# Kernel tuning notes

Hardware: AMD Instinct MI355X
Metric: run time of the kernel (lower is better)

## Reference

```python
import jax, jax.numpy as jnp
import numpy as np
from jax import lax

C = 256
POOL = 7
NUM_CLASSES = 81
D = NUM_CLASSES - 1
STRIDES = (4, 8, 16, 32)
DEC_MULT = (0.1, 0.1, 0.2, 0.2)  # decode_settings: multipliers on raw deltas
LOG_MAX = float(np.log(1000.0 / 16.0))


def setup_inputs() -> dict:
    key = jax.random.key(0)
    ks = jax.random.split(key, 16)
    n, Rp = 2, 512
    R = n * Rp
    img = 800.0
    cx = jax.random.uniform(ks[0], (R,), minval=0.0, maxval=img)
    cy = jax.random.uniform(ks[1], (R,), minval=0.0, maxval=img)
    w = jax.random.uniform(ks[2], (R,), minval=16.0, maxval=300.0)
    h = jax.random.uniform(ks[3], (R,), minval=16.0, maxval=300.0)
    x1 = jnp.clip(cx - w / 2, 0.0, img - 1.0)
    y1 = jnp.clip(cy - h / 2, 0.0, img - 1.0)
    x2 = jnp.minimum(jnp.maximum(cx + w / 2, x1 + 1.0), img)
    y2 = jnp.minimum(jnp.maximum(cy + h / 2, y1 + 1.0), img)
    proposals = jnp.stack([x1, y1, x2, y2], -1)
    imidx = jnp.repeat(jnp.arange(n, dtype=jnp.int32), Rp)
    fmaps = {}
    for li, s in enumerate(STRIDES):
        hw = int(800 // s)
        fmaps[f"fmap{li}"] = jax.random.normal(ks[4 + li], (n, hw, hw, C), jnp.float32)
    c1, clin = C * POOL * POOL, 1024
    def lin(k, fi, fo):
        return (jax.random.normal(k, (fi, fo), jnp.float32) / np.sqrt(fi).astype(np.float32),
                jnp.zeros((fo,), jnp.float32))
    W0, b0 = lin(ks[8], c1, clin)
    W1, b1 = lin(ks[9], clin, clin)
    Wc, bc = lin(ks[10], clin, NUM_CLASSES)
    Wr, br = lin(ks[11], clin, NUM_CLASSES * 4)
    imsizes = jnp.full((n, 2), img, jnp.float32)  # (h, w) per image
    return dict(proposals=proposals, imidx=imidx, **fmaps,
                W0=W0, b0=b0, W1=W1, b1=b1, Wc=Wc, bc=bc, Wr=Wr, br=br,
                imsizes=imsizes, score_thr=0.05, iou_thr=0.5, imtop=100, min_size=1.0)


def _roi_align_level(fmap, boxes, imidx, stride):
    # fmap [n,H,W,C], boxes [R,4] xyxy in image coords; 1 sample per bin, bilinear.
    n, H, W, c = fmap.shape
    s = 1.0 / stride
    x1, y1, x2, y2 = boxes[:, 0] * s, boxes[:, 1] * s, boxes[:, 2] * s, boxes[:, 3] * s
    g = (jnp.arange(POOL, dtype=jnp.float32) + 0.5) / POOL  # bin centers in [0,1]
    xs = x1[:, None] + g[None, :] * (x2 - x1)[:, None] - 0.5  # [R,POOL]
    ys = y1[:, None] + g[None, :] * (y2 - y1)[:, None] - 0.5
    R = boxes.shape[0]
    xx = jnp.broadcast_to(xs[:, None, :], (R, POOL, POOL))
    yy = jnp.broadcast_to(ys[:, :, None], (R, POOL, POOL))
    x0f, y0f = jnp.floor(xx), jnp.floor(yy)
    wx, wy = xx - x0f, yy - y0f
    x0 = jnp.clip(x0f.astype(jnp.int32), 0, W - 1)
    x1i = jnp.clip(x0f.astype(jnp.int32) + 1, 0, W - 1)
    y0 = jnp.clip(y0f.astype(jnp.int32), 0, H - 1)
    y1i = jnp.clip(y0f.astype(jnp.int32) + 1, 0, H - 1)
    ii = imidx[:, None, None]
    v00 = fmap[ii, y0, x0]; v01 = fmap[ii, y0, x1i]
    v10 = fmap[ii, y1i, x0]; v11 = fmap[ii, y1i, x1i]  # each [R,POOL,POOL,C]
    wx, wy = wx[..., None], wy[..., None]
    return (v00 * (1 - wx) * (1 - wy) + v01 * wx * (1 - wy)
            + v10 * (1 - wx) * wy + v11 * wx * wy)


def _forward(proposals, imidx, fmaps, W0, b0, W1, b1, Wc, bc, Wr, br,
             imsizes, score_thr, iou_thr, imtop, min_size):
    R = proposals.shape[0]
    pw = proposals[:, 2] - proposals[:, 0]
    ph = proposals[:, 3] - proposals[:, 1]
    # FPN level assignment (torchvision canonical formula)
    lvl = jnp.floor(4.0 + jnp.log2(jnp.sqrt(pw * ph) / 224.0 + 1e-6))
    lvl = jnp.clip(lvl, 2, 5).astype(jnp.int32) - 2
    pooled = jnp.zeros((R, POOL, POOL, C), fmaps[0].dtype)
    for k, (fm, st) in enumerate(zip(fmaps, STRIDES)):
        pk = _roi_align_level(fm, proposals, imidx, st)
        pooled = jnp.where((lvl == k)[:, None, None, None], pk, pooled)
    # two-FC head + cls/reg
    x = pooled.reshape(R, -1)
    x = jax.nn.relu(x @ W0 + b0)
    x = jax.nn.relu(x @ W1 + b1)
    reg = (x @ Wr + br).reshape(R, NUM_CLASSES, 4)[:, 1:]      # [R,D,4]
    scr = jax.nn.softmax(x @ Wc + bc, axis=-1)[:, 1:]          # [R,D]
    cls = jnp.broadcast_to(jnp.arange(1, NUM_CLASSES, dtype=jnp.int32), (R, D))
    # decode boxes (proposal cwh + weighted deltas, log-space clamp)
    cx = (proposals[:, 0] + proposals[:, 2]) * 0.5
    cy = (proposals[:, 1] + proposals[:, 3]) * 0.5
    dx = reg[..., 0] * DEC_MULT[0]
    dy = reg[..., 1] * DEC_MULT[1]
    dw = jnp.minimum(reg[..., 2] * DEC_MULT[2], LOG_MAX)
    dh = jnp.minimum(reg[..., 3] * DEC_MULT[3], LOG_MAX)
    ncx = dx * pw[:, None] + cx[:, None]
    ncy = dy * ph[:, None] + cy[:, None]
    nw = jnp.exp(dw) * pw[:, None]
    nh = jnp.exp(dh) * ph[:, None]
    hb = imsizes[imidx, 0][:, None]
    wb = imsizes[imidx, 1][:, None]
    bx1 = jnp.clip(ncx - nw / 2, 0.0, wb); bx2 = jnp.clip(ncx + nw / 2, 0.0, wb)
    by1 = jnp.clip(ncy - nh / 2, 0.0, hb); by2 = jnp.clip(ncy + nh / 2, 0.0, hb)
    boxes = jnp.stack([bx1, by1, bx2, by2], -1)                # [R,D,4]
    valid = (scr > score_thr) & (bx2 - bx1 >= min_size) & (by2 - by1 >= min_size)
    # flatten roi-class pairs; class-offset boxes = torchvision batched_nms trick
    M = R * D
    boxes_f = boxes.reshape(M, 4)
    scr_f = scr.reshape(M)
    cls_f = cls.reshape(M)
    valid_f = valid.reshape(M)
    imidx_f = jnp.repeat(imidx, D)
    off = cls_f.astype(boxes_f.dtype)[:, None] * (jnp.max(imsizes) + 2.0)
    bo = boxes_f + off
    areas = (bo[:, 2] - bo[:, 0]) * (bo[:, 3] - bo[:, 1])
    def nms(scores0):
        def step(scores, _):
            i = jnp.argmax(scores)
            s = scores[i]
            b = bo[i]
            iw = jnp.clip(jnp.minimum(b[2], bo[:, 2]) - jnp.maximum(b[0], bo[:, 0]), 0.0)
            ih = jnp.clip(jnp.minimum(b[3], bo[:, 3]) - jnp.maximum(b[1], bo[:, 1]), 0.0)
            inter = iw * ih
            iou = inter / (areas[i] + areas - inter + 1e-6)
            scores = jnp.where(iou > iou_thr, -1.0, scores)
            scores = scores.at[i].set(-1.0)
            return scores, (i, s)
        _, (idx, s) = lax.scan(step, scores0, None, length=imtop)
        return idx, s
    n = imsizes.shape[0]
    ob, osc, ocl = [], [], []
    for i in range(n):
        s0 = jnp.where(valid_f & (imidx_f == i), scr_f, -1.0)
        idx, s = nms(s0)
        keep = s > 0.0  # padded slots have score <= 0
        ob.append(jnp.where(keep[:, None], boxes_f[idx], 0.0))
        osc.append(jnp.where(keep, s, 0.0))
        ocl.append(jnp.where(keep, cls_f[idx], -1))
    return jnp.stack(ob), jnp.stack(osc), jnp.stack(ocl)


def reference(proposals, imidx, fmap0, fmap1, fmap2, fmap3, W0, b0, W1, b1,
              Wc, bc, Wr, br, imsizes, score_thr, iou_thr, imtop, min_size):
    return _forward(proposals, imidx, (fmap0, fmap1, fmap2, fmap3), W0, b0, W1,
                    b1, Wc, bc, Wr, br, imsizes, score_thr, iou_thr, int(imtop),
                    min_size)
```

## Files before the change

kernel.cpp:

```cpp
#include <hip/hip_runtime.h>
#include <math.h>

#define CCH 256
#define NPOOL 7
#define NCLS 81
#define DCLS 80
#define NHEAD 512
#define FLOG_MAX 4.1351666f

typedef _Float16 half8 __attribute__((ext_vector_type(8)));
typedef _Float16 half4 __attribute__((ext_vector_type(4)));
typedef float floatx4 __attribute__((ext_vector_type(4)));

__global__ void zero_k(float4* __restrict__ p, int count4)
{
    int i = blockIdx.x * blockDim.x + threadIdx.x;
    if (i < count4) p[i] = make_float4(0.f, 0.f, 0.f, 0.f);
}

__device__ __forceinline__ void roi_setup(
    const float* __restrict__ prop, const int* __restrict__ imidx,
    const float* __restrict__ f0, const float* __restrict__ f1,
    const float* __restrict__ f2, const float* __restrict__ f3,
    int h0, int h1, int h2, int h3, int b,
    const float*& base, int& W, size_t& o00, size_t& o01, size_t& o10, size_t& o11,
    float& w00, float& w01, float& w10, float& w11)
{
    int roi = b / 49, p = b % 49;
    int py = p / 7, px = p % 7;

    const float* pr = prop + (size_t)roi * 4;
    float x1 = pr[0], y1 = pr[1], x2 = pr[2], y2 = pr[3];
    float pw = x2 - x1, ph = y2 - y1;

    float lv = floorf(4.0f + log2f(sqrtf(pw * ph) / 224.0f + 1e-6f));
    lv = fminf(fmaxf(lv, 2.0f), 5.0f);
    int lvl = (int)lv - 2;

    const float* fm; int H; float s;
    if (lvl == 0)      { fm = f0; H = h0; s = 0.25f;    }
    else if (lvl == 1) { fm = f1; H = h1; s = 0.125f;   }
    else if (lvl == 2) { fm = f2; H = h2; s = 0.0625f;  }
    else               { fm = f3; H = h3; s = 0.03125f; }
    W = H;

    float xs1 = x1 * s, ys1 = y1 * s, xs2 = x2 * s, ys2 = y2 * s;
    float gx = (px + 0.5f) / 7.0f, gy = (py + 0.5f) / 7.0f;
    float xx = xs1 + gx * (xs2 - xs1) - 0.5f;
    float yy = ys1 + gy * (ys2 - ys1) - 0.5f;
    float x0f = floorf(xx), y0f = floorf(yy);
    float wx = xx - x0f, wy = yy - y0f;
    int x0i = min(max((int)x0f, 0), W - 1);
    int x1i = min(max((int)x0f + 1, 0), W - 1);
    int y0i = min(max((int)y0f, 0), H - 1);
    int y1i = min(max((int)y0f + 1, 0), H - 1);

    int ii = imidx[roi];
    base = fm + (size_t)ii * H * W * CCH;
    o00 = ((size_t)y0i * W + x0i) * CCH;
    o01 = ((size_t)y0i * W + x1i) * CCH;
    o10 = ((size_t)y1i * W + x0i) * CCH;
    o11 = ((size_t)y1i * W + x1i) * CCH;
    w00 = (1.0f - wx) * (1.0f - wy);
    w01 = wx * (1.0f - wy);
    w10 = (1.0f - wx) * wy;
    w11 = wx * wy;
}

__global__ void roi_align_k(const float* __restrict__ prop,
                            const int* __restrict__ imidx,
                            const float* __restrict__ f0,
                            const float* __restrict__ f1,
                            const float* __restrict__ f2,
                            const float* __restrict__ f3,
                            int h0, int h1, int h2, int h3,
                            float* __restrict__ pooled)
{
    int b = blockIdx.x, c = threadIdx.x;
    const float* base; int W; size_t o00, o01, o10, o11;
    float w00, w01, w10, w11;
    roi_setup(prop, imidx, f0, f1, f2, f3, h0, h1, h2, h3, b,
              base, W, o00, o01, o10, o11, w00, w01, w10, w11);
    float v = base[o00 + c] * w00 + base[o01 + c] * w01
            + base[o10 + c] * w10 + base[o11 + c] * w11;
    pooled[(size_t)b * CCH + c] = v;
}

__global__ __launch_bounds__(256) void roi_align_f16v4_k(
    const float* __restrict__ prop, const int* __restrict__ imidx,
    const float* __restrict__ f0, const float* __restrict__ f1,
    const float* __restrict__ f2, const float* __restrict__ f3,
    int h0, int h1, int h2, int h3,
    _Float16* __restrict__ poolH, _Float16* __restrict__ poolL)
{
    int b = blockIdx.x * 4 + (threadIdx.x >> 6);
    int lane = threadIdx.x & 63;
    const float* base; int W; size_t o00, o01, o10, o11;
    float w00, w01, w10, w11;
    roi_setup(prop, imidx, f0, f1, f2, f3, h0, h1, h2, h3, b,
              base, W, o00, o01, o10, o11, w00, w01, w10, w11);

    int c4 = lane * 4;
    float4 v00 = *(const float4*)(base + o00 + c4);
    float4 v01 = *(const float4*)(base + o01 + c4);
    float4 v10 = *(const float4*)(base + o10 + c4);
    float4 v11 = *(const float4*)(base + o11 + c4);
    const float* p00 = (const float*)&v00;
    const float* p01 = (const float*)&v01;
    const float* p10 = (const float*)&v10;
    const float* p11 = (const float*)&v11;

    half4 h, l;
#pragma unroll
    for (int e = 0; e < 4; ++e) {
        float v = p00[e] * w00 + p01[e] * w01 + p10[e] * w10 + p11[e] * w11;
        _Float16 hh = (_Float16)v;
        h[e] = hh;
        l[e] = (_Float16)(v - (float)hh);
    }
    size_t idx = (size_t)b * CCH + c4;
    *(half4*)(poolH + idx) = h;
    *(half4*)(poolL + idx) = l;
}

__global__ __launch_bounds__(256) void convert_w_t_k(const float* __restrict__ W,
                                                     _Float16* __restrict__ WtH,
                                                     _Float16* __restrict__ WtL,
                                                     int K, int N)
{
    __shared__ float sh[64][65];
    int k0 = blockIdx.x * 64, n0 = blockIdx.y * 64;
    int t = threadIdx.x;
#pragma unroll
    for (int p = 0; p < 4; ++p) {
        int idx = p * 256 + t;
        int kr = idx >> 4, nc = (idx & 15) * 4;
        float4 v = *(const float4*)(W + (size_t)(k0 + kr) * N + n0 + nc);
        sh[kr][nc + 0] = v.x; sh[kr][nc + 1] = v.y;
        sh[kr][nc + 2] = v.z; sh[kr][nc + 3] = v.w;
    }
    __syncthreads();
#pragma unroll
    for (int p = 0; p < 4; ++p) {
        int idx = p * 256 + t;
        int nr = idx >> 4, kc = (idx & 15) * 4;
        half4 h, l;
#pragma unroll
        for (int i = 0; i < 4; ++i) {
            float v = sh[kc + i][nr];
            _Float16 hh = (_Float16)v;
            h[i] = hh;
            l[i] = (_Float16)(v - (float)hh);
        }
        *(half4*)(WtH + (size_t)(n0 + nr) * K + k0 + kc) = h;
        *(half4*)(WtL + (size_t)(n0 + nr) * K + k0 + kc) = l;
    }
}

__global__ __launch_bounds__(256) void convert_w_t_guard_k(const float* __restrict__ W,
                                                           _Float16* __restrict__ WtH,
                                                           _Float16* __restrict__ WtL,
                                                           int K, int N, int Kt, int rowofs)
{
    __shared__ float sh[64][65];
    int k0 = blockIdx.x * 64, n0 = blockIdx.y * 64;
    int t = threadIdx.x;
#pragma unroll
    for (int p = 0; p < 4; ++p) {
        int idx = p * 256 + t;
        int kr = idx >> 4, nc = (idx & 15) * 4;
#pragma unroll
        for (int e = 0; e < 4; ++e) {
            int nn = n0 + nc + e;
            sh[kr][nc + e] = (nn < N) ? W[(size_t)(k0 + kr) * N + nn] : 0.0f;
        }
    }
    __syncthreads();
#pragma unroll
    for (int p = 0; p < 4; ++p) {
        int idx = p * 256 + t;
        int nr = idx >> 4, kc = (idx & 15) * 4;
        if (n0 + nr < N) {
            half4 h, l;
#pragma unroll
            for (int i = 0; i < 4; ++i) {
                float v = sh[kc + i][nr];
                _Float16 hh = (_Float16)v;
                h[i] = hh;
                l[i] = (_Float16)(v - (float)hh);
            }
            *(half4*)(WtH + (size_t)(rowofs + n0 + nr) * Kt + k0 + kc) = h;
            *(half4*)(WtL + (size_t)(rowofs + n0 + nr) * Kt + k0 + kc) = l;
        }
    }
}

__global__ void act_split_k(const float* __restrict__ acc,
                            const float* __restrict__ bias,
                            _Float16* __restrict__ outH,
                            _Float16* __restrict__ outL,
                            int total, int CL)
{
    int i = (blockIdx.x * blockDim.x + threadIdx.x) * 4;
    if (i >= total) return;
    int b = i % CL;
    float4 v = *(const float4*)(acc + i);
    float4 bb = *(const float4*)(bias + b);
    const float* pv = (const float*)&v;
    const float* pb = (const float*)&bb;
    half4 h, l;
#pragma unroll
    for (int e = 0; e < 4; ++e) {
        float f = fmaxf(pv[e] + pb[e], 0.0f);
        _Float16 hh = (_Float16)f;
        h[e] = hh;
        l[e] = (_Float16)(f - (float)hh);
    }
    *(half4*)(outH + i) = h;
    *(half4*)(outL + i) = l;
}

__device__ __forceinline__ void dma16(const _Float16* g, _Float16* l)
{
    __builtin_amdgcn_global_load_lds(
        (const __attribute__((address_space(1))) unsigned int*)g,
        (__attribute__((address_space(3))) unsigned int*)l, 16, 0, 0);
}

#define LDKE 32

__global__ __launch_bounds__(256) void gemm_mfma_split_k(
    const _Float16* __restrict__ Ah, const _Float16* __restrict__ Al,
    const _Float16* __restrict__ Bh, const _Float16* __restrict__ Bl,
    float* __restrict__ Cacc, int M, int N, int K, int Kc, int SP)
{
    __shared__ _Float16 sAh[128 * LDKE], sAl[128 * LDKE];
    __shared__ _Float16 sBh[128 * LDKE], sBl[128 * LDKE];

    int bid = blockIdx.x;
    int z = bid % SP;
    int q = bid / SP;
    int NT = N >> 7;
    int nn = q % NT;
    int m = q / NT;
    int m0 = m * 128, n0 = nn * 128;
    int kb = z * Kc;
    int ke = min(K, kb + Kc);

    int t = threadIdx.x;
    int lane = t & 63, w = t >> 6;
    int wr = w >> 1, wc = w & 1;
    int fr = lane & 15;
    int fk = (lane >> 4) * 8;

    int drow = w * 32 + (lane >> 2);
    int dkq = (lane & 3) * 8;
    const _Float16* gAh = Ah + (size_t)(m0 + drow) * K + dkq;
    const _Float16* gAl = Al + (size_t)(m0 + drow) * K + dkq;
    const _Float16* gBh = Bh + (size_t)(n0 + drow) * K + dkq;
    const _Float16* gBl = Bl + (size_t)(n0 + drow) * K + dkq;
    size_t rowskip = (size_t)16 * K;

    _Float16* lAh0 = &sAh[(w * 2 + 0) * 512];
    _Float16* lAh1 = &sAh[(w * 2 + 1) * 512];
    _Float16* lAl0 = &sAl[(w * 2 + 0) * 512];
    _Float16* lAl1 = &sAl[(w * 2 + 1) * 512];
    _Float16* lBh0 = &sBh[(w * 2 + 0) * 512];
    _Float16* lBh1 = &sBh[(w * 2 + 1) * 512];
    _Float16* lBl0 = &sBl[(w * 2 + 0) * 512];
    _Float16* lBl1 = &sBl[(w * 2 + 1) * 512];

    floatx4 acc[4][4] = {};

    for (int k0 = kb; k0 < ke; k0 += 32) {
        dma16(gAh + k0, lAh0);
        dma16(gAh + rowskip + k0, lAh1);
        dma16(gAl + k0, lAl0);
        dma16(gAl + rowskip + k0, lAl1);
        dma16(gBh + k0, lBh0);
        dma16(gBh + rowskip + k0, lBh1);
        dma16(gBl + k0, lBl0);
        dma16(gBl + rowskip + k0, lBl1);
        __syncthreads();

        half8 ah[4], al[4], bh[4], bl[4];
#pragma unroll
        for (int i = 0; i < 4; ++i) {
            int ar = wr * 64 + i * 16 + fr;
            ah[i] = *(const half8*)&sAh[ar * LDKE + fk];
            al[i] = *(const half8*)&sAl[ar * LDKE + fk];
            int bc = wc * 64 + i * 16 + fr;
            bh[i] = *(const half8*)&sBh[bc * LDKE + fk];
            bl[i] = *(const half8*)&sBl[bc * LDKE + fk];
        }
#pragma unroll
        for (int i = 0; i < 4; ++i)
#pragma unroll
            for (int j = 0; j < 4; ++j) {
                acc[i][j] = __builtin_amdgcn_mfma_f32_16x16x32_f16(ah[i], bh[j], acc[i][j], 0, 0, 0);
                acc[i][j] = __builtin_amdgcn_mfma_f32_16x16x32_f16(ah[i], bl[j], acc[i][j], 0, 0, 0);
                acc[i][j] = __builtin_amdgcn_mfma_f32_16x16x32_f16(al[i], bh[j], acc[i][j], 0, 0, 0);
            }
        __syncthreads();
    }

    int rbase = (lane >> 4) * 4;
#pragma unroll
    for (int i = 0; i < 4; ++i)
#pragma unroll
        for (int j = 0; j < 4; ++j) {
            int col = n0 + wc * 64 + j * 16 + fr;
#pragma unroll
            for (int r = 0; r < 4; ++r) {
                int row = m0 + wr * 64 + i * 16 + rbase + r;
                atomicAdd(&Cacc[(size_t)row * N + col], acc[i][j][r]);
            }
        }
}

__global__ __launch_bounds__(256) void gemm_mfma_fused64_k(
    const _Float16* __restrict__ Ah, const _Float16* __restrict__ Al,
    const _Float16* __restrict__ Bh, const _Float16* __restrict__ Bl,
    const float* __restrict__ bias,
    float* __restrict__ Cout,
    _Float16* __restrict__ outH, _Float16* __restrict__ outL,
    int M, int N, int K, int mode)
{
    __shared__ _Float16 sAh[2][64 * LDKE], sAl[2][64 * LDKE];
    __shared__ _Float16 sBh[2][64 * LDKE], sBl[2][64 * LDKE];

    int m0 = blockIdx.y * 64, n0 = blockIdx.x * 64;
    int t = threadIdx.x;
    int lane = t & 63, w = t >> 6;
    int wr = w >> 1, wc = w & 1;
    int fr = lane & 15;
    int fk = (lane >> 4) * 8;

    int drow = w * 16 + (lane >> 2);
    int dkq = (lane & 3) * 8;
    const _Float16* gAh = Ah + (size_t)(m0 + drow) * K + dkq;
    const _Float16* gAl = Al + (size_t)(m0 + drow) * K + dkq;
    const _Float16* gBh = Bh + (size_t)(n0 + drow) * K + dkq;
    const _Float16* gBl = Bl + (size_t)(n0 + drow) * K + dkq;
    int lofs = w * 512;

    int nt = K >> 5;

    dma16(gAh + 0, &sAh[0][lofs]);
    dma16(gAl + 0, &sAl[0][lofs]);
    dma16(gBh + 0, &sBh[0][lofs]);
    dma16(gBl + 0, &sBl[0][lofs]);
    __syncthreads();

    floatx4 acc[2][2] = {};

    for (int tt = 0; tt < nt; ++tt) {
        int c = tt & 1, nb = c ^ 1;
        if (tt + 1 < nt) {
            int k1 = (tt + 1) << 5;
            dma16(gAh + k1, &sAh[nb][lofs]);
            dma16(gAl + k1, &sAl[nb][lofs]);
            dma16(gBh + k1, &sBh[nb][lofs]);
            dma16(gBl + k1, &sBl[nb][lofs]);
        }

        half8 ah[2], av[2], bh[2], bv[2];
#pragma unroll
        for (int i = 0; i < 2; ++i) {
            int ar = wr * 32 + i * 16 + fr;
            ah[i] = *(const half8*)&sAh[c][ar * LDKE + fk];
            av[i] = *(const half8*)&sAl[c][ar * LDKE + fk];
            int bc = wc * 32 + i * 16 + fr;
            bh[i] = *(const half8*)&sBh[c][bc * LDKE + fk];
            bv[i] = *(const half8*)&sBl[c][bc * LDKE + fk];
        }
#pragma unroll
        for (int i = 0; i < 2; ++i)
#pragma unroll
            for (int j = 0; j < 2; ++j) {
                acc[i][j] = __builtin_amdgcn_mfma_f32_16x16x32_f16(ah[i], bh[j], acc[i][j], 0, 0, 0);
                acc[i][j] = __builtin_amdgcn_mfma_f32_16x16x32_f16(ah[i], bv[j], acc[i][j], 0, 0, 0);
                acc[i][j] = __builtin_amdgcn_mfma_f32_16x16x32_f16(av[i], bh[j], acc[i][j], 0, 0, 0);
            }
        __syncthreads();
    }

    int rbase = (lane >> 4) * 4;
#pragma unroll
    for (int i = 0; i < 2; ++i)
#pragma unroll
        for (int j = 0; j < 2; ++j) {
            int col = n0 + wc * 32 + j * 16 + fr;
#pragma unroll
            for (int r = 0; r < 4; ++r) {
                int row = m0 + wr * 32 + i * 16 + rbase + r;
                float v = acc[i][j][r];
                if (mode == 0) {
                    Cout[(size_t)row * N + col] = v;
                } else {
                    float f = fmaxf(v + bias[col], 0.0f);
                    _Float16 hh = (_Float16)f;
                    outH[(size_t)row * N + col] = hh;
                    outL[(size_t)row * N + col] = (_Float16)(f - (float)hh);
                }
            }
        }
}

__global__ __launch_bounds__(256) void gemm_splitk_k(const float* __restrict__ A,
                                                     const float* __restrict__ B,
                                                     const float* __restrict__ abias,
                                                     float* __restrict__ Cacc,
                                                     int M, int N, int K, int Kc)
{
    __shared__ float Ast[16][68];
    __shared__ float Bs[16][68];

    int m0 = blockIdx.y * 64, n0 = blockIdx.x * 64;
    int kb = blockIdx.z * Kc;
    int ke = min(K, kb + Kc);
    int tid = threadIdx.x;
    int tx = tid & 15, ty = tid >> 4;
    int arow = tid >> 2, akq = (tid & 3) << 2;
    int bcol = tid & 63, bk = tid >> 6;

    const float* Arow = A + (size_t)(m0 + arow) * K;
    bool nfull = (n0 + 64 <= N);

    float acc[4][4] = {};

    for (int k0 = kb; k0 < ke; k0 += 16) {
        float4 av = *(const float4*)(Arow + k0 + akq);
        if (abias) {
            av.x = fmaxf(av.x + abias[k0 + akq + 0], 0.0f);
            av.y = fmaxf(av.y + abias[k0 + akq + 1], 0.0f);
            av.z = fmaxf(av.z + abias[k0 + akq + 2], 0.0f);
            av.w = fmaxf(av.w + abias[k0 + akq + 3], 0.0f);
        }
        float bv[4];
        if (nfull) {
#pragma unroll
            for (int e = 0; e < 4; ++e)
                bv[e] = B[(size_t)(k0 + bk * 4 + e) * N + n0 + bcol];
        } else {
            bool ok = (n0 + bcol) < N;
#pragma unroll
            for (int e = 0; e < 4; ++e)
                bv[e] = ok ? B[(size_t)(k0 + bk * 4 + e) * N + n0 + bcol] : 0.0f;
        }
        __syncthreads();
        Ast[akq + 0][arow] = av.x;
        Ast[akq + 1][arow] = av.y;
        Ast[akq + 2][arow] = av.z;
        Ast[akq + 3][arow] = av.w;
#pragma unroll
        for (int e = 0; e < 4; ++e) Bs[bk * 4 + e][bcol] = bv[e];
        __syncthreads();

#pragma unroll
        for (int kk = 0; kk < 16; ++kk) {
            float4 af = *(const float4*)&Ast[kk][ty * 4];
            float4 bf = *(const float4*)&Bs[kk][tx * 4];
            float a_[4] = {af.x, af.y, af.z, af.w};
            float b_[4] = {bf.x, bf.y, bf.z, bf.w};
#pragma unroll
            for (int i = 0; i < 4; ++i)
#pragma unroll
                for (int j = 0; j < 4; ++j)
                    acc[i][j] = fmaf(a_[i], b_[j], acc[i][j]);
        }
    }

#pragma unroll
    for (int i = 0; i < 4; ++i) {
        int row = m0 + ty * 4 + i;
#pragma unroll
        for (int j = 0; j < 4; ++j) {
            int col = n0 + tx * 4 + j;
            if (col < N) atomicAdd(&Cacc[(size_t)row * N + col], acc[i][j]);
        }
    }
}

__global__ void softmax_k(const float* __restrict__ logits, int ldl,
                          const float* __restrict__ bc,
                          float* __restrict__ scr)
{
    int r = blockIdx.x;
    int t = threadIdx.x;
    const float* row = logits + (size_t)r * ldl;

    float v0 = row[t] + bc[t];
    float v1 = (t + 64 < NCLS) ? (row[t + 64] + bc[t + 64]) : -INFINITY;
    float m = fmaxf(v0, v1);
#pragma unroll
    for (int o = 32; o > 0; o >>= 1) m = fmaxf(m, __shfl_down(m, o));
    m = __shfl(m, 0);

    float e0 = expf(v0 - m);
    float e1 = (t + 64 < NCLS) ? expf(v1 - m) : 0.0f;
    float sum = e0 + e1;
#pragma unroll
    for (int o = 32; o > 0; o >>= 1) sum += __shfl_down(sum, o);
    sum = __shfl(sum, 0);
    float inv = 1.0f / sum;

    if (t >= 1)        scr[(size_t)r * DCLS + (t - 1)]  = e0 * inv;
    if (t + 64 < NCLS) scr[(size_t)r * DCLS + (t + 63)] = e1 * inv;
}

#define NMS_T 1024
#define NMS_CPT 8
__global__ __launch_bounds__(NMS_T) void nms_k(
    const float* __restrict__ scr,
    const float* __restrict__ prop,
    const int* __restrict__ imidx,
    const float* __restrict__ head, int ldh, int regofs,
    const float* __restrict__ br,
    const float* __restrict__ imsz,
    const float* __restrict__ score_thr_p,
    const float* __restrict__ min_size_p,
    const float* __restrict__ iou_thr_p,
    int* __restrict__ cidx,
    float* __restrict__ cscore,
    float* __restrict__ cbo,
    float* __restrict__ cbox,
    float* __restrict__ carea,
    float* __restrict__ out,
    int M, int n, int imtop)
{
    int img = blockIdx.x;
    int t = threadIdx.x;
    const int T = NMS_T;
    const int NW = NMS_T / 64;
    int lane = t & 63, wid = t >> 6;

    __shared__ int cnt;
    __shared__ float ws_sc[NW], ws_o0[NW], ws_o1[NW], ws_o2[NW], ws_o3[NW], ws_ar[NW];
    __shared__ int ws_g[NW], ws_p[NW];
    __shared__ float f_sc, f_o0, f_o1, f_o2, f_o3, f_ar;
    __shared__ int f_g, f_p;

    if (t == 0) cnt = 0;
    __syncthreads();

    float score_thr = score_thr_p[0];
    float min_size  = min_size_p[0];
    float iou_thr   = iou_thr_p[0];
    float immax = imsz[0];
    for (int q = 1; q < 2 * n; ++q) immax = fmaxf(immax, imsz[q]);

    int base = img * M;
    for (int j = t; j < M; j += T) {
        int r = j / DCLS;
        if (imidx[r] != img) continue;
        float s = scr[j];
        if (s <= score_thr) continue;

        int cls = j - r * DCLS + 1;
        const float* pr = prop + (size_t)r * 4;
        float pw = pr[2] - pr[0], ph = pr[3] - pr[1];
        float cx = (pr[0] + pr[2]) * 0.5f, cy = (pr[1] + pr[3]) * 0.5f;
        const float* rg_ = head + (size_t)r * ldh + regofs + cls * 4;
        const float* bb = br + cls * 4;
        float dx = (rg_[0] + bb[0]) * 0.1f;
        float dy = (rg_[1] + bb[1]) * 0.1f;
        float dw = fminf((rg_[2] + bb[2]) * 0.2f, FLOG_MAX);
        float dh = fminf((rg_[3] + bb[3]) * 0.2f, FLOG_MAX);
        float ncx = dx * pw + cx;
        float ncy = dy * ph + cy;
        float nw = expf(dw) * pw;
        float nh = expf(dh) * ph;
        float hbound = imsz[img * 2 + 0];
        float wbound = imsz[img * 2 + 1];
        float bx1 = fminf(fmaxf(ncx - nw * 0.5f, 0.0f), wbound);
        float bx2 = fminf(fmaxf(ncx + nw * 0.5f, 0.0f), wbound);
        float by1 = fminf(fmaxf(ncy - nh * 0.5f, 0.0f), hbound);
        float by2 = fminf(fmaxf(ncy + nh * 0.5f, 0.0f), hbound);
        if (bx2 - bx1 < min_size || by2 - by1 < min_size) continue;

        float off = (float)cls * (immax + 2.0f);
        int p = atomicAdd(&cnt, 1);
        cidx[base + p] = j;
        cscore[base + p] = s;
        cbox[(size_t)(base + p) * 4 + 0] = bx1;
        cbox[(size_t)(base + p) * 4 + 1] = by1;
        cbox[(size_t)(base + p) * 4 + 2] = bx2;
        cbox[(size_t)(base + p) * 4 + 3] = by2;
        cbo[(size_t)(base + p) * 4 + 0] = bx1 + off;
        cbo[(size_t)(base + p) * 4 + 1] = by1 + off;
        cbo[(size_t)(base + p) * 4 + 2] = bx2 + off;
        cbo[(size_t)(base + p) * 4 + 3] = by2 + off;
        carea[base + p] = (bx2 - bx1) * (by2 - by1);
    }
    __syncthreads();
    int K = cnt;

    float* ob  = out;
    float* osc = out + (size_t)n * imtop * 4;
    float* ocl = out + (size_t)n * imtop * 5;

    int it = 0;
    if (K <= T * NMS_CPT) {
        float rsc[NMS_CPT], ro0[NMS_CPT], ro1[NMS_CPT], ro2[NMS_CPT], ro3[NMS_CPT], rar[NMS_CPT];
        int rgi[NMS_CPT];
#pragma unroll
        for (int s = 0; s < NMS_CPT; ++s) {
            int p = t + s * T;
            bool ok = p < K;
            rsc[s] = ok ? cscore[base + p] : -1e30f;
            rgi[s] = ok ? cidx[base + p] : 0x7fffffff;
            ro0[s] = ok ? cbo[(size_t)(base + p) * 4 + 0] : 0.0f;
            ro1[s] = ok ? cbo[(size_t)(base + p) * 4 + 1] : 0.0f;
            ro2[s] = ok ? cbo[(size_t)(base + p) * 4 + 2] : 0.0f;
            ro3[s] = ok ? cbo[(size_t)(base + p) * 4 + 3] : 0.0f;
            rar[s] = ok ? carea[base + p] : 0.0f;
        }

        for (; it < imtop; ++it) {
            float bsc = -1e30f; int bg = 0x7fffffff, bp = -1;
            float b0 = 0.f, b1 = 0.f, b2 = 0.f, b3 = 0.f, ba = 0.f;
#pragma unroll
            for (int s = 0; s < NMS_CPT; ++s) {
                if (rsc[s] > bsc || (rsc[s] == bsc && rgi[s] < bg)) {
                    bsc = rsc[s]; bg = rgi[s]; bp = t + s * T;
                    b0 = ro0[s]; b1 = ro1[s]; b2 = ro2[s]; b3 = ro3[s]; ba = rar[s];
                }
            }
#pragma unroll
            for (int o = 32; o > 0; o >>= 1) {
                float os = __shfl_down(bsc, o);
                int   og = __shfl_down(bg, o);
                int   op = __shfl_down(bp, o);
                float q0 = __shfl_down(b0, o), q1 = __shfl_down(b1, o);
                float q2 = __shfl_down(b2, o), q3 = __shfl_down(b3, o);
                float qa = __shfl_down(ba, o);
                if (os > bsc || (os == bsc && og < bg)) {
                    bsc = os; bg = og; bp = op;
                    b0 = q0; b1 = q1; b2 = q2; b3 = q3; ba = qa;
                }
            }
            if (lane == 0) {
                ws_sc[wid] = bsc; ws_g[wid] = bg; ws_p[wid] = bp;
                ws_o0[wid] = b0; ws_o1[wid] = b1; ws_o2[wid] = b2; ws_o3[wid] = b3;
                ws_ar[wid] = ba;
            }
            __syncthreads();
            if (wid == 0) {
                float s2 = (lane < NW) ? ws_sc[lane] : -1e30f;
                int   g2 = (lane < NW) ? ws_g[lane] : 0x7fffffff;
                int   p2 = (lane < NW) ? ws_p[lane] : -1;
                float c0 = (lane < NW) ? ws_o0[lane] : 0.f;
                float c1 = (lane < NW) ? ws_o1[lane] : 0.f;
                float c2 = (lane < NW) ? ws_o2[lane] : 0.f;
                float c3 = (lane < NW) ? ws_o3[lane] : 0.f;
                float ca = (lane < NW) ? ws_ar[lane] : 0.f;
#pragma unroll
                for (int o = NW / 2; o > 0; o >>= 1) {
                    float os = __shfl_down(s2, o);
                    int   og = __shfl_down(g2, o);
                    int   op = __shfl_down(p2, o);
                    float q0 = __shfl_down(c0, o), q1 = __shfl_down(c1, o);
                    float q2 = __shfl_down(c2, o), q3 = __shfl_down(c3, o);
                    float qa = __shfl_down(ca, o);
                    if (os > s2 || (os == s2 && og < g2)) {
                        s2 = os; g2 = og; p2 = op;
                        c0 = q0; c1 = q1; c2 = q2; c3 = q3; ca = qa;
                    }
                }
                if (lane == 0) {
                    f_sc = s2; f_g = g2; f_p = p2;
                    f_o0 = c0; f_o1 = c1; f_o2 = c2; f_o3 = c3; f_ar = ca;
                }
            }
            __syncthreads();
            float wsc = f_sc;
            if (wsc <= 0.0f) break;
            float w0 = f_o0, w1 = f_o1, w2 = f_o2, w3 = f_o3, wa = f_ar;
            int wp = f_p, wg = f_g;

#pragma unroll
            for (int s = 0; s < NMS_CPT; ++s) {
                if (t + s * T == wp) {
                    size_t oslot = (size_t)img * imtop + it;
                    ob[oslot * 4 + 0] = cbox[(size_t)(base + wp) * 4 + 0];
                    ob[oslot * 4 + 1] = cbox[(size_t)(base + wp) * 4 + 1];
                    ob[oslot * 4 + 2] = cbox[(size_t)(base + wp) * 4 + 2];
                    ob[oslot * 4 + 3] = cbox[(size_t)(base + wp) * 4 + 3];
                    osc[oslot] = wsc;
                    ocl[oslot] = (float)(wg % DCLS + 1);
                    rsc[s] = -1e30f;
                }
            }
#pragma unroll
            for (int s = 0; s < NMS_CPT; ++s) {
                float iw = fmaxf(fminf(w2, ro2[s]) - fmaxf(w0, ro0[s]), 0.0f);
                float ih = fmaxf(fminf(w3, ro3[s]) - fmaxf(w1, ro1[s]), 0.0f);
                float inter = iw * ih;
                float iou = inter / (wa + rar[s] - inter + 1e-6f);
                if (iou > iou_thr) rsc[s] = -1e30f;
            }
        }
    } else {
        for (; it < imtop; ++it) {
            float best = -1e30f; int bg = 0x7fffffff; int bl = -1;
            for (int p = t; p < K; p += T) {
                float sv = cscore[base + p];
                int g = cidx[base + p];
                if (sv > best || (sv == best && g < bg)) { best = sv; bg = g; bl = p; }
            }
#pragma unroll
            for (int o = 32; o > 0; o >>= 1) {
                float os = __shfl_down(best, o);
                int   og = __shfl_down(bg, o);
                int   ol = __shfl_down(bl, o);
                if (os > best || (os == best && og < bg)) { best = os; bg = og; bl = ol; }
            }
            if (lane == 0) { ws_sc[wid] = best; ws_g[wid] = bg; ws_p[wid] = bl; }
            __syncthreads();
            if (wid == 0) {
                float b2 = (lane < NW) ? ws_sc[lane] : -1e30f;
                int   g2 = (lane < NW) ? ws_g[lane] : 0x7fffffff;
                int   l2 = (lane < NW) ? ws_p[lane] : -1;
#pragma unroll
                for (int o = NW / 2; o > 0; o >>= 1) {
                    float os = __shfl_down(b2, o);
                    int   og = __shfl_down(g2, o);
                    int   ol = __shfl_down(l2, o);
                    if (os > b2 || (os == b2 && og < g2)) { b2 = os; g2 = og; l2 = ol; }
                }
                if (lane == 0) {
                    f_sc = b2;
                    if (b2 > 0.0f) {
                        int lp = l2;
                        size_t oslot = (size_t)img * imtop + it;
                        ob[oslot * 4 + 0] = cbox[(size_t)(base + lp) * 4 + 0];
                        ob[oslot * 4 + 1] = cbox[(size_t)(base + lp) * 4 + 1];
                        ob[oslot * 4 + 2] = cbox[(size_t)(base + lp) * 4 + 2];
                        ob[oslot * 4 + 3] = cbox[(size_t)(base + lp) * 4 + 3];
                        osc[oslot] = b2;
                        ocl[oslot] = (float)(g2 % DCLS + 1);
                        f_o0 = cbo[(size_t)(base + lp) * 4 + 0];
                        f_o1 = cbo[(size_t)(base + lp) * 4 + 1];
                        f_o2 = cbo[(size_t)(base + lp) * 4 + 2];
                        f_o3 = cbo[(size_t)(base + lp) * 4 + 3];
                        f_ar = carea[base + lp];
                        cscore[base + lp] = -1.0f;
                    }
                }
            }
            __syncthreads();
            if (f_sc <= 0.0f) break;

            float b0 = f_o0, b1 = f_o1, b2_ = f_o2, b3 = f_o3, ai = f_ar;
            for (int p = t; p < K; p += T) {
                float c0 = cbo[(size_t)(base + p) * 4 + 0];
                float c1 = cbo[(size_t)(base + p) * 4 + 1];
                float c2 = cbo[(size_t)(base + p) * 4 + 2];
                float c3 = cbo[(size_t)(base + p) * 4 + 3];
                float iw = fmaxf(fminf(b2_, c2) - fmaxf(b0, c0), 0.0f);
                float ih = fmaxf(fminf(b3, c3) - fmaxf(b1, c1), 0.0f);
                float inter = iw * ih;
                float iou = inter / (ai + carea[base + p] - inter + 1e-6f);
                if (iou > iou_thr) cscore[base + p] = -1.0f;
            }
            __syncthreads();
        }
    }

    for (int q = it + t; q < imtop; q += T) {
        size_t oslot = (size_t)img * imtop + q;
        ob[oslot * 4 + 0] = 0.0f;
        ob[oslot * 4 + 1] = 0.0f;
        ob[oslot * 4 + 2] = 0.0f;
        ob[oslot * 4 + 3] = 0.0f;
        osc[oslot] = 0.0f;
        ocl[oslot] = -1.0f;
    }
}

extern "C" void kernel_launch(void* const* d_in, const int* in_sizes, int n_in,
                              void* d_out, int out_size, void* d_ws, size_t ws_size,
                              hipStream_t stream)
{
    const float* prop   = (const float*)d_in[0];
    const int*   imidx  = (const int*)d_in[1];
    const float* f0     = (const float*)d_in[2];
    const float* f1     = (const float*)d_in[3];
    const float* f2     = (const float*)d_in[4];
    const float* f3     = (const float*)d_in[5];
    const float* W0     = (const float*)d_in[6];
    const float* b0     = (const float*)d_in[7];
    const float* W1     = (const float*)d_in[8];
    const float* b1     = (const float*)d_in[9];
    const float* Wc     = (const float*)d_in[10];
    const float* bc     = (const float*)d_in[11];
    const float* Wr     = (const float*)d_in[12];
    const float* br     = (const float*)d_in[13];
    const float* imsz   = (const float*)d_in[14];
    const float* sthr   = (const float*)d_in[15];
    const float* ithr   = (const float*)d_in[16];
    const float* msz    = (const float*)d_in[18];

    int R = in_sizes[1];
    int n = in_sizes[14] / 2;
    int imtop = out_size / (n * 6);
    int M = R * DCLS;
    int K0 = NPOOL * NPOOL * CCH;
    int CL = in_sizes[7];

    int h0 = (int)(sqrtf((float)(in_sizes[2] / (n * CCH))) + 0.5f);
    int h1 = (int)(sqrtf((float)(in_sizes[3] / (n * CCH))) + 0.5f);
    int h2 = (int)(sqrtf((float)(in_sizes[4] / (n * CCH))) + 0.5f);
    int h3 = (int)(sqrtf((float)(in_sizes[5] / (n * CCH))) + 0.5f);

    float* outf = (float*)d_out;

    size_t szPool  = (size_t)R * K0 * 2;
    size_t szX     = (size_t)R * CL * 4;
    size_t szHead  = (size_t)R * NHEAD * 4;
    size_t szWh    = (size_t)NHEAD * CL * 2;
    size_t szXh    = (size_t)R * CL * 2;
    size_t szW1t   = (size_t)CL * CL * 2;
    size_t szScr   = (size_t)R * DCLS * 4;

    size_t needed = 4 * szPool + 2 * szX + szHead + 2 * szWh
                  + 4 * szXh + 2 * szW1t + szScr;

    int splitK0 = 8;
    bool mfma_ok = (ws_size >= needed) && (R % 128 == 0) && (CL % 128 == 0)
                 && (K0 % (splitK0 * 32) == 0) && (CL % 32 == 0)
                 && ((R * 49) % 4 == 0);

    if (mfma_ok) {
        uint8_t* w = (uint8_t*)d_ws;
        size_t o = 0;
        _Float16* poolH   = (_Float16*)(w + o); o += szPool;
        _Float16* poolL   = (_Float16*)(w + o); o += szPool;
        _Float16* W0tH    = (_Float16*)(w + o); o += szPool;
        _Float16* W0tL    = (_Float16*)(w + o); o += szPool;
        float*    x0acc   = (float*)(w + o);    o += szX;
        float*    unused  = (float*)(w + o);    o += szX;
        float*    headacc = (float*)(w + o);    o += szHead;
        _Float16* WheadtH = (_Float16*)(w + o); o += szWh;
        _Float16* WheadtL = (_Float16*)(w + o); o += szWh;
        _Float16* x0H     = (_Float16*)(w + o); o += szXh;
        _Float16* x0L     = (_Float16*)(w + o); o += szXh;
        _Float16* x1H     = (_Float16*)(w + o); o += szXh;
        _Float16* x1L     = (_Float16*)(w + o); o += szXh;
        _Float16* W1tH    = (_Float16*)(w + o); o += szW1t;
        _Float16* W1tL    = (_Float16*)(w + o); o += szW1t;
        float*    scr     = (float*)(w + o);
        (void)unused;

        int*   cidx   = (int*)d_ws;
        float* cscore = (float*)(cidx + (size_t)n * M);
        float* cbo    = cscore + (size_t)n * M;
        float* cbox   = cbo + (size_t)n * M * 4;
        float* carea  = cbox + (size_t)n * M * 4;

        {
            int c4 = (int)(szX / 16);
            zero_k<<<dim3((c4 + 255) / 256), dim3(256), 0, stream>>>((float4*)x0acc, c4);
        }
        convert_w_t_k<<<dim3(K0 / 64, CL / 64), dim3(256), 0, stream>>>(W0, W0tH, W0tL, K0, CL);
        convert_w_t_k<<<dim3(CL / 64, CL / 64), dim3(256), 0, stream>>>(W1, W1tH, W1tL, CL, CL);
        convert_w_t_guard_k<<<dim3(CL / 64, (NCLS + 63) / 64), dim3(256), 0, stream>>>(
            Wc, WheadtH, WheadtL, CL, NCLS, CL, 0);
        convert_w_t_guard_k<<<dim3(CL / 64, (NCLS * 4 + 63) / 64), dim3(256), 0, stream>>>(
            Wr, WheadtH, WheadtL, CL, NCLS * 4, CL, NCLS);
        roi_align_f16v4_k<<<dim3(R * 49 / 4), dim3(256), 0, stream>>>(
            prop, imidx, f0, f1, f2, f3, h0, h1, h2, h3, poolH, poolL);
        gemm_mfma_split_k<<<dim3(splitK0 * (R / 128) * (CL / 128)), dim3(256), 0, stream>>>(
            poolH, poolL, W0tH, W0tL, x0acc, R, CL, K0, K0 / splitK0, splitK0);
        act_split_k<<<dim3((R * CL / 4 + 255) / 256), dim3(256), 0, stream>>>(
            x0acc, b0, x0H, x0L, R * CL, CL);
        gemm_mfma_fused64_k<<<dim3(CL / 64, R / 64), dim3(256), 0, stream>>>(
            x0H, x0L, W1tH, W1tL, b1, nullptr, x1H, x1L, R, CL, CL, 1);
        gemm_mfma_fused64_k<<<dim3(NHEAD / 64, R / 64), dim3(256), 0, stream>>>(
            x1H, x1L, WheadtH, WheadtL, nullptr, headacc, nullptr, nullptr, R, NHEAD, CL, 0);
        softmax_k<<<dim3(R), dim3(64), 0, stream>>>(headacc, NHEAD, bc, scr);
        nms_k<<<dim3(n), dim3(NMS_T), 0, stream>>>(
            scr, prop, imidx, headacc, NHEAD, NCLS, br, imsz, sthr, msz, ithr,
            cidx, cscore, cbo, cbox, carea, outf, M, n, imtop);
    } else {
        float* ws = (float*)d_ws;
        size_t off = 0;
        float* pooled  = ws + off; off += (size_t)R * K0;
        float* x0acc   = ws + off; off += (size_t)R * CL;
        float* x1acc   = ws + off; off += (size_t)R * CL;
        float* logits  = ws + off; off += (size_t)R * NCLS;
        off = (off + 3) & ~(size_t)3;
        float* reg     = ws + off; off += (size_t)R * NCLS * 4;
        float* scr     = ws + off; off += (size_t)R * DCLS;

        int*   cidx   = (int*)ws;
        float* cscore = (float*)(cidx + (size_t)n * M);
        float* cbo    = cscore + (size_t)n * M;
        float* cbox   = cbo + (size_t)n * M * 4;
        float* carea  = cbox + (size_t)n * M * 4;

        {
            size_t zcount = (size_t)(reg + (size_t)R * NCLS * 4 - x0acc);
            int c4 = (int)(zcount / 4);
            zero_k<<<dim3((c4 + 255) / 256), dim3(256), 0, stream>>>((float4*)x0acc, c4);
        }
        roi_align_k<<<dim3(R * 49), dim3(256), 0, stream>>>(
            prop, imidx, f0, f1, f2, f3, h0, h1, h2, h3, pooled);
        gemm_splitk_k<<<dim3(CL / 64, R / 64, 8), dim3(256), 0, stream>>>(
            pooled, W0, nullptr, x0acc, R, CL, K0, 1568);
        gemm_splitk_k<<<dim3(CL / 64, R / 64, 4), dim3(256), 0, stream>>>(
            x0acc, W1, b0, x1acc, R, CL, CL, 256);
        gemm_splitk_k<<<dim3((NCLS + 63) / 64, R / 64, 8), dim3(256), 0, stream>>>(
            x1acc, Wc, b1, logits, R, NCLS, CL, 128);
        gemm_splitk_k<<<dim3((NCLS * 4 + 63) / 64, R / 64, 4), dim3(256), 0, stream>>>(
            x1acc, Wr, b1, reg, R, NCLS * 4, CL, 256);
        softmax_k<<<dim3(R), dim3(64), 0, stream>>>(logits, NCLS, bc, scr);
        nms_k<<<dim3(n), dim3(NMS_T), 0, stream>>>(
            scr, prop, imidx, reg, NCLS * 4, 0, br, imsz, sthr, msz, ithr,
            cidx, cscore, cbo, cbox, carea, outf, M, n, imtop);
    }
}
```

Measured before the change: 421.9 us.

## Replace iterative argmax NMS with bitonic sort plus single-wave greedy suppression; swizzle LDS

The NMS kernel used to run up to imtop block-wide argmax reductions, each followed by two __syncthreads. It now bitonic-sorts the candidate keys (score, then inverted index) in shared memory and lets one wavefront walk the sorted list in chunks of 64. Each chunk is checked against the already-accepted boxes, and the survivors are accepted in order through ballot and shuffle. This trades many block syncs for a sort whose cost grows with K, and leaves only one wave doing the greedy pass. The GEMM kernels also get an XOR swizzle on the LDS k-offsets, aimed at reducing bank conflicts.

New measurement: 419.4 us. No clear change (-0.6%).

```diff
diff --git a/kernel.cpp b/kernel.cpp
--- a/kernel.cpp
+++ b/kernel.cpp
@@ -228,6 +228,8 @@
 }
 
 #define LDKE 32
+#define DKQ_SWZ(lane)  ((((lane) & 3) ^ (((lane) >> 3) & 3)) << 3)
+#define FK_SWZ(lane)   (((((lane) >> 4) ^ (((lane) >> 1) & 3))) << 3)
 
 __global__ __launch_bounds__(256) void gemm_mfma_split_k(
     const _Float16* __restrict__ Ah, const _Float16* __restrict__ Al,
@@ -251,10 +253,10 @@
     int lane = t & 63, w = t >> 6;
     int wr = w >> 1, wc = w & 1;
     int fr = lane & 15;
-    int fk = (lane >> 4) * 8;
+    int fk = FK_SWZ(lane);
 
     int drow = w * 32 + (lane >> 2);
-    int dkq = (lane & 3) * 8;
+    int dkq = DKQ_SWZ(lane);
     const _Float16* gAh = Ah + (size_t)(m0 + drow) * K + dkq;
     const _Float16* gAl = Al + (size_t)(m0 + drow) * K + dkq;
     const _Float16* gBh = Bh + (size_t)(n0 + drow) * K + dkq;
@@ -334,10 +336,10 @@
     int lane = t & 63, w = t >> 6;
     int wr = w >> 1, wc = w & 1;
     int fr = lane & 15;
-    int fk = (lane >> 4) * 8;
+    int fk = FK_SWZ(lane);
 
     int drow = w * 16 + (lane >> 2);
-    int dkq = (lane & 3) * 8;
+    int dkq = DKQ_SWZ(lane);
     const _Float16* gAh = Ah + (size_t)(m0 + drow) * K + dkq;
     const _Float16* gAl = Al + (size_t)(m0 + drow) * K + dkq;
     const _Float16* gBh = Bh + (size_t)(n0 + drow) * K + dkq;
@@ -510,7 +512,8 @@
 }
 
 #define NMS_T 1024
-#define NMS_CPT 8
+#define NMS_SORTMAX 4096
+#define NMS_AMAX 512
 __global__ __launch_bounds__(NMS_T) void nms_k(
     const float* __restrict__ scr,
     const float* __restrict__ prop,
@@ -536,10 +539,13 @@
     int lane = t & 63, wid = t >> 6;
 
     __shared__ int cnt;
-    __shared__ float ws_sc[NW], ws_o0[NW], ws_o1[NW], ws_o2[NW], ws_o3[NW], ws_ar[NW];
+    __shared__ unsigned long long skey[NMS_SORTMAX];
+    __shared__ int sp_[NMS_SORTMAX];
+    __shared__ float aab0[NMS_AMAX], aab1[NMS_AMAX], aab2[NMS_AMAX], aab3[NMS_AMAX], aaa[NMS_AMAX];
+    __shared__ int f_it;
+    __shared__ float ws_sc[NW];
     __shared__ int ws_g[NW], ws_p[NW];
     __shared__ float f_sc, f_o0, f_o1, f_o2, f_o3, f_ar;
-    __shared__ int f_g, f_p;
 
     if (t == 0) cnt = 0;
     __syncthreads();
@@ -601,106 +607,101 @@
     float* ocl = out + (size_t)n * imtop * 5;
 
     int it = 0;
-    if (K <= T * NMS_CPT) {
-        float rsc[NMS_CPT], ro0[NMS_CPT], ro1[NMS_CPT], ro2[NMS_CPT], ro3[NMS_CPT], rar[NMS_CPT];
-        int rgi[NMS_CPT];
-#pragma unroll
-        for (int s = 0; s < NMS_CPT; ++s) {
-            int p = t + s * T;
-            bool ok = p < K;
-            rsc[s] = ok ? cscore[base + p] : -1e30f;
-            rgi[s] = ok ? cidx[base + p] : 0x7fffffff;
-            ro0[s] = ok ? cbo[(size_t)(base + p) * 4 + 0] : 0.0f;
-            ro1[s] = ok ? cbo[(size_t)(base + p) * 4 + 1] : 0.0f;
-            ro2[s] = ok ? cbo[(size_t)(base + p) * 4 + 2] : 0.0f;
-            ro3[s] = ok ? cbo[(size_t)(base + p) * 4 + 3] : 0.0f;
-            rar[s] = ok ? carea[base + p] : 0.0f;
-        }
-
-        for (; it < imtop; ++it) {
-            float bsc = -1e30f; int bg = 0x7fffffff, bp = -1;
-            float b0 = 0.f, b1 = 0.f, b2 = 0.f, b3 = 0.f, ba = 0.f;
-#pragma unroll
-            for (int s = 0; s < NMS_CPT; ++s) {
-                if (rsc[s] > bsc || (rsc[s] == bsc && rgi[s] < bg)) {
-                    bsc = rsc[s]; bg = rgi[s]; bp = t + s * T;
-                    b0 = ro0[s]; b1 = ro1[s]; b2 = ro2[s]; b3 = ro3[s]; ba = rar[s];
-                }
-            }
-#pragma unroll
-            for (int o = 32; o > 0; o >>= 1) {
-                float os = __shfl_down(bsc, o);
-                int   og = __shfl_down(bg, o);
-                int   op = __shfl_down(bp, o);
-                float q0 = __shfl_down(b0, o), q1 = __shfl_down(b1, o);
-                float q2 = __shfl_down(b2, o), q3 = __shfl_down(b3, o);
-                float qa = __shfl_down(ba, o);
-                if (os > bsc || (os == bsc && og < bg)) {
-                    bsc = os; bg = og; bp = op;
-                    b0 = q0; b1 = q1; b2 = q2; b3 = q3; ba = qa;
-                }
-            }
-            if (lane == 0) {
-                ws_sc[wid] = bsc; ws_g[wid] = bg; ws_p[wid] = bp;
-                ws_o0[wid] = b0; ws_o1[wid] = b1; ws_o2[wid] = b2; ws_o3[wid] = b3;
-                ws_ar[wid] = ba;
-            }
-            __syncthreads();
-            if (wid == 0) {
-                float s2 = (lane < NW) ? ws_sc[lane] : -1e30f;
-                int   g2 = (lane < NW) ? ws_g[lane] : 0x7fffffff;
-                int   p2 = (lane < NW) ? ws_p[lane] : -1;
-                float c0 = (lane < NW) ? ws_o0[lane] : 0.f;
-                float c1 = (lane < NW) ? ws_o1[lane] : 0.f;
-                float c2 = (lane < NW) ? ws_o2[lane] : 0.f;
-                float c3 = (lane < NW) ? ws_o3[lane] : 0.f;
-                float ca = (lane < NW) ? ws_ar[lane] : 0.f;
-#pragma unroll
-                for (int o = NW / 2; o > 0; o >>= 1) {
-                    float os = __shfl_down(s2, o);
-                    int   og = __shfl_down(g2, o);
-                    int   op = __shfl_down(p2, o);
-                    float q0 = __shfl_down(c0, o), q1 = __shfl_down(c1, o);
-                    float q2 = __shfl_down(c2, o), q3 = __shfl_down(c3, o);
-                    float qa = __shfl_down(ca, o);
-                    if (os > s2 || (os == s2 && og < g2)) {
-                        s2 = os; g2 = og; p2 = op;
-                        c0 = q0; c1 = q1; c2 = q2; c3 = q3; ca = qa;
+    if (K <= NMS_SORTMAX && imtop <= NMS_AMAX) {
+        int SN = 64; while (SN < K) SN <<= 1;
+        for (int i = t; i < SN; i += T) {
+            if (i < K) {
+                unsigned int sb = __float_as_uint(cscore[base + i]);
+                skey[i] = ((unsigned long long)sb << 32)
+                        | (unsigned int)(~cidx[base + i]);
+            } else {
+                skey[i] = 0ull;
+            }
+            sp_[i] = i;
+        }
+        for (int k = 2; k <= SN; k <<= 1) {
+            for (int j = k >> 1; j > 0; j >>= 1) {
+                __syncthreads();
+                for (int i = t; i < SN; i += T) {
+                    int l = i ^ j;
+                    if (l > i) {
+                        unsigned long long ki = skey[i], kl = skey[l];
+                        bool up = ((i & k) == 0);
+                        bool sw = up ? (ki < kl) : (ki > kl);
+                        if (sw) {
+                            skey[i] = kl; skey[l] = ki;
+                            int tp = sp_[i]; sp_[i] = sp_[l]; sp_[l] = tp;
+                        }
                     }
                 }
-                if (lane == 0) {
-                    f_sc = s2; f_g = g2; f_p = p2;
-                    f_o0 = c0; f_o1 = c1; f_o2 = c2; f_o3 = c3; f_ar = ca;
+            }
+        }
+        __syncthreads();
+
+        if (wid == 0) {
+            int na = 0;
+            for (int c0 = 0; c0 < K && na < imtop; c0 += 64) {
+                int ci = c0 + lane;
+                bool alive = ci < K;
+                float x0 = 0.f, x1 = 0.f, x2 = 0.f, x3 = 0.f, ar_ = 0.f, sc = 0.f;
+                float q0 = 0.f, q1 = 0.f, q2 = 0.f, q3 = 0.f;
+                int g = 0;
+                if (alive) {
+                    unsigned long long key = skey[ci];
+                    sc = __uint_as_float((unsigned int)(key >> 32));
+                    int pp = sp_[ci];
+                    g = cidx[base + pp];
+                    x0 = cbo[(size_t)(base + pp) * 4 + 0];
+                    x1 = cbo[(size_t)(base + pp) * 4 + 1];
+                    x2 = cbo[(size_t)(base + pp) * 4 + 2];
+                    x3 = cbo[(size_t)(base + pp) * 4 + 3];
+                    ar_ = carea[base + pp];
+                    q0 = cbox[(size_t)(base + pp) * 4 + 0];
+                    q1 = cbox[(size_t)(base + pp) * 4 + 1];
+                    q2 = cbox[(size_t)(base + pp) * 4 + 2];
+                    q3 = cbox[(size_t)(base + pp) * 4 + 3];
+                    if (sc <= 0.0f) alive = false;
                 }
-            }
-            __syncthreads();
-            float wsc = f_sc;
-            if (wsc <= 0.0f) break;
-            float w0 = f_o0, w1 = f_o1, w2 = f_o2, w3 = f_o3, wa = f_ar;
-            int wp = f_p, wg = f_g;
-
-#pragma unroll
-            for (int s = 0; s < NMS_CPT; ++s) {
-                if (t + s * T == wp) {
-                    size_t oslot = (size_t)img * imtop + it;
-                    ob[oslot * 4 + 0] = cbox[(size_t)(base + wp) * 4 + 0];
-                    ob[oslot * 4 + 1] = cbox[(size_t)(base + wp) * 4 + 1];
-                    ob[oslot * 4 + 2] = cbox[(size_t)(base + wp) * 4 + 2];
-                    ob[oslot * 4 + 3] = cbox[(size_t)(base + wp) * 4 + 3];
-                    osc[oslot] = wsc;
-                    ocl[oslot] = (float)(wg % DCLS + 1);
-                    rsc[s] = -1e30f;
+                for (int a = 0; a < na; ++a) {
+                    float iw = fmaxf(fminf(aab2[a], x2) - fmaxf(aab0[a], x0), 0.0f);
+                    float ih = fmaxf(fminf(aab3[a], x3) - fmaxf(aab1[a], x1), 0.0f);
+                    float inter = iw * ih;
+                    float iou = inter / (aaa[a] + ar_ - inter + 1e-6f);
+                    if (iou > iou_thr) alive = false;
                 }
-            }
-#pragma unroll
-            for (int s = 0; s < NMS_CPT; ++s) {
-                float iw = fmaxf(fminf(w2, ro2[s]) - fmaxf(w0, ro0[s]), 0.0f);
-                float ih = fmaxf(fminf(w3, ro3[s]) - fmaxf(w1, ro1[s]), 0.0f);
-                float inter = iw * ih;
-                float iou = inter / (wa + rar[s] - inter + 1e-6f);
-                if (iou > iou_thr) rsc[s] = -1e30f;
-            }
-        }
+                unsigned long long mm = __ballot(alive);
+                while (mm != 0ull && na < imtop) {
+                    int s = __ffsll(mm) - 1;
+                    float b0 = __shfl(x0, s), b1 = __shfl(x1, s);
+                    float b2v = __shfl(x2, s), b3v = __shfl(x3, s);
+                    float ba = __shfl(ar_, s);
+                    if (lane == s) {
+                        size_t oslot = (size_t)img * imtop + na;
+                        ob[oslot * 4 + 0] = q0;
+                        ob[oslot * 4 + 1] = q1;
+                        ob[oslot * 4 + 2] = q2;
+                        ob[oslot * 4 + 3] = q3;
+                        osc[oslot] = sc;
+                        ocl[oslot] = (float)(g % DCLS + 1);
+                        aab0[na] = x0; aab1[na] = x1; aab2[na] = x2; aab3[na] = x3;
+                        aaa[na] = ar_;
+                        alive = false;
+                    }
+                    na++;
+                    if (alive && lane > s) {
+                        float iw = fmaxf(fminf(b2v, x2) - fmaxf(b0, x0), 0.0f);
+                        float ih = fmaxf(fminf(b3v, x3) - fmaxf(b1, x1), 0.0f);
+                        float inter = iw * ih;
+                        float iou = inter / (ba + ar_ - inter + 1e-6f);
+                        if (iou > iou_thr) alive = false;
+                    }
+                    mm = __ballot(alive);
+                }
+            }
+            if (lane == 0) f_it = na;
+        }
+        __syncthreads();
+        it = f_it;
     } else {
         for (; it < imtop; ++it) {
             float best = -1e30f; int bg = 0x7fffffff; int bl = -1;
```
